# Optimization experiments

Hardware: AMD Instinct MI355X
Metric: run time of the kernel (lower is better)

The kernel has to match this reference:

```python
import jax, jax.numpy as jnp
import numpy as np

EMBED_DIM = 1024
NUM_HEADS = 16
HEAD_DIM = EMBED_DIM // NUM_HEADS
SCALING = HEAD_DIM ** -0.5


def setup_inputs() -> dict:
    key = jax.random.key(0)
    ks = jax.random.split(key, 10)
    B, S, D = 2, 2048, EMBED_DIM
    lim = 1.0 / np.sqrt(D)  # torch Linear default init scale
    def lin(k):
        kw, kb = jax.random.split(k)
        W = jax.random.uniform(kw, (D, D), jnp.float32, -lim, lim)
        b = jax.random.uniform(kb, (D,), jnp.float32, -lim, lim)
        return W, b
    Wq, bq = lin(ks[0])
    Wk, bk = lin(ks[1])
    Wv, bv = lin(ks[2])
    Wo, bo = lin(ks[3])
    hidden_states = jax.random.normal(ks[4], (B, S, D), jnp.float32)
    attention_mask = jnp.ones((B, S), jnp.int32)  # unused by the module's forward
    return {"hidden_states": hidden_states, "attention_mask": attention_mask,
            "Wq": Wq, "bq": bq, "Wk": Wk, "bk": bk, "Wv": Wv, "bv": bv,
            "Wo": Wo, "bo": bo}


def reference(hidden_states, attention_mask, Wq, bq, Wk, bk, Wv, bv, Wo, bo):
    B, S, D = hidden_states.shape
    H, hd = NUM_HEADS, HEAD_DIM

    def split_heads(x):  # [B,S,D] -> [B,H,S,hd]
        return x.reshape(B, S, H, hd).transpose(0, 2, 1, 3)

    q = split_heads(hidden_states @ Wq.T + bq) * SCALING
    k = split_heads(hidden_states @ Wk.T + bk)
    v = split_heads(hidden_states @ Wv.T + bv)

    scores = jnp.einsum("bhqd,bhkd->bhqk", q, k)  # [B,H,S,S]
    mask_value = jnp.finfo(scores.dtype).min
    causal = jnp.triu(jnp.ones((S, S), bool), k=1)  # True above diagonal
    scores = jnp.where(causal, mask_value, scores)
    probs = jax.nn.softmax(scores, axis=-1)

    out = jnp.einsum("bhqk,bhkd->bhqd", probs, v)  # [B,H,S,hd]
    out = out.transpose(0, 2, 1, 3).reshape(B, S, D)
    return out @ Wo.T + bo
```

## Files before the change

kernel.cpp:

```cpp
#include <hip/hip_runtime.h>


typedef __bf16 bf16;
typedef __attribute__((ext_vector_type(8))) __bf16 bf16x8;
typedef __attribute__((ext_vector_type(4))) __bf16 bf16x4;
typedef __attribute__((ext_vector_type(4))) float f32x4;

#define MFMA16(a, b, c) __builtin_amdgcn_mfma_f32_16x16x32_bf16((a), (b), (c), 0, 0, 0)

__device__ __forceinline__ void gl_lds16(const bf16* g, bf16* l) {
  __builtin_amdgcn_global_load_lds(
      (__attribute__((address_space(1))) void*)g,
      (__attribute__((address_space(3))) void*)l, 16, 0, 0);
}

__device__ __forceinline__ float exp2_raw(float x) {
  float r;
  asm("v_exp_f32 %0, %1" : "=v"(r) : "v"(x));
  return r;
}

__global__ __launch_bounds__(256) void cvt5(
    const float* __restrict__ x, const float* __restrict__ wq,
    const float* __restrict__ wk, const float* __restrict__ wv,
    const float* __restrict__ wo,
    bf16* __restrict__ xb, bf16* __restrict__ wqb, bf16* __restrict__ wkb,
    bf16* __restrict__ wvb, bf16* __restrict__ wob) {
  const int bx = blockIdx.x;
  const float* s;
  bf16* d;
  int base;
  if (bx < 4096)      { s = x;  d = xb;  base = bx; }
  else if (bx < 5120) { s = wq; d = wqb; base = bx - 4096; }
  else if (bx < 6144) { s = wk; d = wkb; base = bx - 5120; }
  else if (bx < 7168) { s = wv; d = wvb; base = bx - 6144; }
  else                { s = wo; d = wob; base = bx - 7168; }
  const int i = base * 1024 + threadIdx.x * 4;
  const float4 v = *(const float4*)(s + i);
  bf16x4 o;
  o[0] = (bf16)v.x; o[1] = (bf16)v.y; o[2] = (bf16)v.z; o[3] = (bf16)v.w;
  *(bf16x4*)(d + i) = o;
}

template <int BM, typename OutT>
__global__ __launch_bounds__(256, 2) void gemm_bt3(
    const bf16* __restrict__ A,
    const bf16* __restrict__ W0, const bf16* __restrict__ W1, const bf16* __restrict__ W2,
    const float* __restrict__ B0, const float* __restrict__ B1, const float* __restrict__ B2,
    OutT* __restrict__ O0, OutT* __restrict__ O1, OutT* __restrict__ O2,
    float s0, float s1, float s2, int K, int vt_which) {
  constexpr int WM = BM / 32;
  __shared__ bf16 As[BM * 64];
  __shared__ bf16 Bs[128 * 64];

  const int t = threadIdx.x;
  const int lane = t & 63;
  const int wv = t >> 6;
  const int wm = wv & 1, wn = wv >> 1;
  const int qd = lane >> 4, ln = lane & 15;

  const int which = blockIdx.x >> 3;
  const bf16* W = (which == 0) ? W0 : (which == 1) ? W1 : W2;
  const float* Bi = (which == 0) ? B0 : (which == 1) ? B1 : B2;
  OutT* O = (which == 0) ? O0 : (which == 1) ? O1 : O2;
  const float scale = (which == 0) ? s0 : (which == 1) ? s1 : s2;

  const int n0 = (blockIdx.x & 7) * 128;
  const int m0 = blockIdx.y * BM;

  f32x4 acc[WM][4] = {};

  for (int k0 = 0; k0 < K; k0 += 64) {
#pragma unroll
    for (int i = 0; i < BM / 32; ++i) {
      const int s = i * 256 + t;
      const int row = s >> 3;
      const int c = (s & 7) ^ (row & 7);
      gl_lds16(A + (size_t)(m0 + row) * K + k0 + c * 8, &As[s * 8]);
    }
#pragma unroll
    for (int i = 0; i < 4; ++i) {
      const int s = i * 256 + t;
      const int row = s >> 3;
      const int c = (s & 7) ^ (row & 7);
      gl_lds16(W + (size_t)(n0 + row) * K + k0 + c * 8, &Bs[s * 8]);
    }
    __syncthreads();

#pragma unroll
    for (int ks = 0; ks < 2; ++ks) {
      bf16x8 af[WM], bw[4];
#pragma unroll
      for (int i = 0; i < WM; ++i) {
        const int r = wm * (BM / 2) + i * 16 + ln;
        af[i] = *(const bf16x8*)&As[r * 64 + (((ks * 4 + qd) ^ (ln & 7)) << 3)];
      }
#pragma unroll
      for (int j = 0; j < 4; ++j) {
        const int r = wn * 64 + j * 16 + ln;
        bw[j] = *(const bf16x8*)&Bs[r * 64 + (((ks * 4 + qd) ^ (ln & 7)) << 3)];
      }
#pragma unroll
      for (int i = 0; i < WM; ++i)
#pragma unroll
        for (int j = 0; j < 4; ++j)
          acc[i][j] = MFMA16(af[i], bw[j], acc[i][j]);
    }
    __syncthreads();
  }

#pragma unroll
  for (int i = 0; i < WM; ++i) {
    const int row = m0 + wm * (BM / 2) + i * 16 + qd * 4;
#pragma unroll
    for (int j = 0; j < 4; ++j) {
      const int col = n0 + wn * 64 + j * 16 + ln;
      const float bias = Bi[col];
      if (which == vt_which) {
        const int bb = row >> 11, ss = row & 2047;
        const int hh = col >> 6, dd = col & 63;
        OutT* dst = O + ((size_t)((bb << 4) + hh) * 64 + dd) * 2048 + ss;
        if constexpr (sizeof(OutT) == 2) {
          bf16x4 pk;
#pragma unroll
          for (int r = 0; r < 4; ++r) pk[r] = (bf16)((acc[i][j][r] + bias) * scale);
          *(bf16x4*)dst = pk;
        } else {
#pragma unroll
          for (int r = 0; r < 4; ++r) dst[r] = (OutT)((acc[i][j][r] + bias) * scale);
        }
      } else {
#pragma unroll
        for (int r = 0; r < 4; ++r) {
          const float v = (acc[i][j][r] + bias) * scale;
          O[(size_t)(row + r) * 1024 + col] = (OutT)v;
        }
      }
    }
  }
}

__global__ __launch_bounds__(256, 4) void attn_causal(
    const bf16* __restrict__ Q, const bf16* __restrict__ Kg,
    const bf16* __restrict__ VT, bf16* __restrict__ Ob) {
  __shared__ bf16 Ks[2][64 * 64];
  __shared__ bf16 Vts[2][64 * 64];
  __shared__ bf16 Ps[4][16 * 64];

  const int t = threadIdx.x;
  const int lane = t & 63;
  const int w = t >> 6;
  const int qd = lane >> 4, ln = lane & 15;

  const int blk = blockIdx.x;
  const int bh = blk & 31;
  const int g = blk >> 5;
  const int a = g & 7, b = g >> 3;
  const int tq = (b == 0) ? (31 - a) : (b == 1) ? (16 + a) : (b == 2) ? (15 - a) : a;
  const int bb = bh >> 4, h = bh & 15;
  const size_t rowbase = (size_t)bb * 2048;
  const bf16* vtb = VT + (size_t)bh * 64 * 2048;

  const int q0 = tq * 64;
  const int nj = tq + 1;

  auto stage = [&](int buf, int j) {
    const bf16* kp = Kg + (rowbase + j * 64) * 1024 + h * 64;
#pragma unroll
    for (int i = 0; i < 2; ++i) {
      const int s = i * 256 + t;
      const int kv = s >> 3;
      const int c = (s & 7) ^ (kv & 7);
      gl_lds16(kp + (size_t)kv * 1024 + c * 8, &Ks[buf][s * 8]);
    }
#pragma unroll
    for (int i = 0; i < 2; ++i) {
      const int s = i * 256 + t;
      const int d = s >> 3;
      const int c = (s & 7) ^ (d & 7);
      gl_lds16(vtb + (size_t)d * 2048 + j * 64 + c * 8, &Vts[buf][s * 8]);
    }
  };

  const bf16* qp = Q + (rowbase + q0 + w * 16) * 1024 + h * 64;
  bf16x8 qf[2];
#pragma unroll
  for (int ks = 0; ks < 2; ++ks)
    qf[ks] = *(const bf16x8*)(qp + (size_t)ln * 1024 + ks * 32 + qd * 8);

  float l_run[4] = {0.f, 0.f, 0.f, 0.f};
  f32x4 accO[4] = {};

  stage(0, 0);

#pragma unroll 1
  for (int j = 0; j < nj; ++j) {
    const int buf = j & 1;
    __syncthreads();
    if (j + 1 < nj) stage(buf ^ 1, j + 1);

    f32x4 accS[4] = {};
    __builtin_amdgcn_s_setprio(1);
#pragma unroll
    for (int ks = 0; ks < 2; ++ks) {
#pragma unroll
      for (int nt = 0; nt < 4; ++nt) {
        const bf16x8 bk = *(const bf16x8*)
            &Ks[buf][(nt * 16 + ln) * 64 + (((ks * 4 + qd) ^ (ln & 7)) << 3)];
        accS[nt] = MFMA16(qf[ks], bk, accS[nt]);
      }
    }
    __builtin_amdgcn_s_setprio(0);

    if (j == nj - 1) {
#pragma unroll
      for (int r = 0; r < 4; ++r) {
        const int row = qd * 4 + r;
        const int qg = q0 + w * 16 + row;
        float sum = 0.f;
#pragma unroll
        for (int nt = 0; nt < 4; ++nt) {
          float p = exp2_raw(accS[nt][r]);
          const int col = nt * 16 + ln;
          if ((j * 64 + col) > qg) p = 0.f;
          sum += p;
          Ps[w][row * 64 + ((((col >> 3) ^ (row & 7))) << 3) + (col & 7)] = (bf16)p;
        }
        l_run[r] += sum;
      }
    } else {
#pragma unroll
      for (int r = 0; r < 4; ++r) {
        const int row = qd * 4 + r;
        float sum = 0.f;
#pragma unroll
        for (int nt = 0; nt < 4; ++nt) {
          const float p = exp2_raw(accS[nt][r]);
          const int col = nt * 16 + ln;
          sum += p;
          Ps[w][row * 64 + ((((col >> 3) ^ (row & 7))) << 3) + (col & 7)] = (bf16)p;
        }
        l_run[r] += sum;
      }
    }

    __builtin_amdgcn_s_setprio(1);
#pragma unroll
    for (int kt = 0; kt < 2; ++kt) {
      const bf16x8 ap = *(const bf16x8*)
          &Ps[w][ln * 64 + (((kt * 4 + qd) ^ (ln & 7)) << 3)];
#pragma unroll
      for (int nt = 0; nt < 4; ++nt) {
        const bf16x8 bv = *(const bf16x8*)
            &Vts[buf][(nt * 16 + ln) * 64 + (((kt * 4 + qd) ^ (ln & 7)) << 3)];
        accO[nt] = MFMA16(ap, bv, accO[nt]);
      }
    }
    __builtin_amdgcn_s_setprio(0);
  }

  bf16* op = Ob + (rowbase + q0 + w * 16) * 1024 + h * 64;
#pragma unroll
  for (int r = 0; r < 4; ++r) {
    float l = l_run[r];
#pragma unroll
    for (int off = 1; off < 16; off <<= 1) l += __shfl_xor(l, off, 64);
    const float inv_l = 1.0f / l;
#pragma unroll
    for (int nt = 0; nt < 4; ++nt)
      op[(size_t)(qd * 4 + r) * 1024 + nt * 16 + ln] = (bf16)(accO[nt][r] * inv_l);
  }
}

extern "C" void kernel_launch(void* const* d_in, const int* in_sizes, int n_in,
                              void* d_out, int out_size, void* d_ws, size_t ws_size,
                              hipStream_t stream) {
  const float* X  = (const float*)d_in[0];
  const float* Wq = (const float*)d_in[2];
  const float* bq = (const float*)d_in[3];
  const float* Wk = (const float*)d_in[4];
  const float* bk = (const float*)d_in[5];
  const float* Wv = (const float*)d_in[6];
  const float* bv = (const float*)d_in[7];
  const float* Wo = (const float*)d_in[8];
  const float* bo = (const float*)d_in[9];
  float* out = (float*)d_out;

  bf16* xb  = (bf16*)d_ws;
  bf16* wqb = xb  + (size_t)4096 * 1024;
  bf16* wkb = wqb + (size_t)1024 * 1024;
  bf16* wvb = wkb + (size_t)1024 * 1024;
  bf16* wob = wvb + (size_t)1024 * 1024;
  bf16* q   = wob + (size_t)1024 * 1024;
  bf16* k   = q   + (size_t)4096 * 1024;
  bf16* vt  = k   + (size_t)4096 * 1024;
  bf16* ao  = xb;

  const float scaling = 0.125f * 1.44269504088896f;

  dim3 blk(256);
  cvt5<<<dim3(8192), blk, 0, stream>>>(X, Wq, Wk, Wv, Wo, xb, wqb, wkb, wvb, wob);
  gemm_bt3<128, bf16><<<dim3(24, 32), blk, 0, stream>>>(
      xb, wqb, wkb, wvb, bq, bk, bv, q, k, vt, scaling, 1.f, 1.f, 1024, 2);
  attn_causal<<<dim3(1024), blk, 0, stream>>>(q, k, vt, ao);
  gemm_bt3<64, float><<<dim3(8, 64), blk, 0, stream>>>(
      ao, wob, wob, wob, bo, bo, bo, out, out, out, 1.f, 1.f, 1.f, 1024, -1);
}
```

Before: 183.8 us.

## Run causal attention as single-wave blocks reading K/V straight into registers

The attention kernel goes from 256-thread blocks, where four waves share double-buffered K and V^T tiles staged in LDS through async global-to-LDS loads, to 64-thread blocks. Each block now handles 16 query rows and loads its K and V^T fragments from global memory directly into registers, so LDS holds only the P tile. The grid grows to 4096 blocks and the heavy-first causal tile ordering is dropped. This removes the block barriers and LDS staging, but each K/V tile is now fetched four times as often through the cache. Load latency is no longer overlapped by the double buffer, and light blocks now launch before heavy ones, which can leave a long tail.

After: 266.7 us. 1.45x slower.

```diff
diff --git a/kernel.cpp b/kernel.cpp
--- a/kernel.cpp
+++ b/kernel.cpp
@@ -140,49 +140,26 @@
   }
 }
 
-__global__ __launch_bounds__(256, 4) void attn_causal(
+__global__ __launch_bounds__(64, 4) void attn_causal(
     const bf16* __restrict__ Q, const bf16* __restrict__ Kg,
     const bf16* __restrict__ VT, bf16* __restrict__ Ob) {
-  __shared__ bf16 Ks[2][64 * 64];
-  __shared__ bf16 Vts[2][64 * 64];
-  __shared__ bf16 Ps[4][16 * 64];
-
-  const int t = threadIdx.x;
-  const int lane = t & 63;
-  const int w = t >> 6;
+  __shared__ bf16 Ps[16 * 64];
+
+  const int lane = threadIdx.x;
   const int qd = lane >> 4, ln = lane & 15;
 
   const int blk = blockIdx.x;
   const int bh = blk & 31;
   const int g = blk >> 5;
-  const int a = g & 7, b = g >> 3;
-  const int tq = (b == 0) ? (31 - a) : (b == 1) ? (16 + a) : (b == 2) ? (15 - a) : a;
   const int bb = bh >> 4, h = bh & 15;
   const size_t rowbase = (size_t)bb * 2048;
+  const bf16* kb = Kg + rowbase * 1024 + h * 64;
   const bf16* vtb = VT + (size_t)bh * 64 * 2048;
 
-  const int q0 = tq * 64;
-  const int nj = tq + 1;
-
-  auto stage = [&](int buf, int j) {
-    const bf16* kp = Kg + (rowbase + j * 64) * 1024 + h * 64;
-#pragma unroll
-    for (int i = 0; i < 2; ++i) {
-      const int s = i * 256 + t;
-      const int kv = s >> 3;
-      const int c = (s & 7) ^ (kv & 7);
-      gl_lds16(kp + (size_t)kv * 1024 + c * 8, &Ks[buf][s * 8]);
-    }
-#pragma unroll
-    for (int i = 0; i < 2; ++i) {
-      const int s = i * 256 + t;
-      const int d = s >> 3;
-      const int c = (s & 7) ^ (d & 7);
-      gl_lds16(vtb + (size_t)d * 2048 + j * 64 + c * 8, &Vts[buf][s * 8]);
-    }
-  };
-
-  const bf16* qp = Q + (rowbase + q0 + w * 16) * 1024 + h * 64;
+  const int q0 = g * 16;
+  const int nj = (g >> 2) + 1;
+
+  const bf16* qp = Q + (rowbase + q0) * 1024 + h * 64;
   bf16x8 qf[2];
 #pragma unroll
   for (int ks = 0; ks < 2; ++ks)
@@ -191,32 +168,38 @@
   float l_run[4] = {0.f, 0.f, 0.f, 0.f};
   f32x4 accO[4] = {};
 
-  stage(0, 0);
-
 #pragma unroll 1
   for (int j = 0; j < nj; ++j) {
-    const int buf = j & 1;
-    __syncthreads();
-    if (j + 1 < nj) stage(buf ^ 1, j + 1);
+    bf16x8 bk[2][4];
+#pragma unroll
+    for (int ks = 0; ks < 2; ++ks)
+#pragma unroll
+      for (int nt = 0; nt < 4; ++nt)
+        bk[ks][nt] = *(const bf16x8*)
+            (kb + (size_t)(j * 64 + nt * 16 + ln) * 1024 + ks * 32 + qd * 8);
 
     f32x4 accS[4] = {};
     __builtin_amdgcn_s_setprio(1);
 #pragma unroll
-    for (int ks = 0; ks < 2; ++ks) {
-#pragma unroll
-      for (int nt = 0; nt < 4; ++nt) {
-        const bf16x8 bk = *(const bf16x8*)
-            &Ks[buf][(nt * 16 + ln) * 64 + (((ks * 4 + qd) ^ (ln & 7)) << 3)];
-        accS[nt] = MFMA16(qf[ks], bk, accS[nt]);
-      }
-    }
+    for (int ks = 0; ks < 2; ++ks)
+#pragma unroll
+      for (int nt = 0; nt < 4; ++nt)
+        accS[nt] = MFMA16(qf[ks], bk[ks][nt], accS[nt]);
     __builtin_amdgcn_s_setprio(0);
+
+    bf16x8 bv[2][4];
+#pragma unroll
+    for (int kt = 0; kt < 2; ++kt)
+#pragma unroll
+      for (int nt = 0; nt < 4; ++nt)
+        bv[kt][nt] = *(const bf16x8*)
+            (vtb + (size_t)(nt * 16 + ln) * 2048 + j * 64 + kt * 32 + qd * 8);
 
     if (j == nj - 1) {
 #pragma unroll
       for (int r = 0; r < 4; ++r) {
         const int row = qd * 4 + r;
-        const int qg = q0 + w * 16 + row;
+        const int qg = q0 + row;
         float sum = 0.f;
 #pragma unroll
         for (int nt = 0; nt < 4; ++nt) {
@@ -224,7 +207,7 @@
           const int col = nt * 16 + ln;
           if ((j * 64 + col) > qg) p = 0.f;
           sum += p;
-          Ps[w][row * 64 + ((((col >> 3) ^ (row & 7))) << 3) + (col & 7)] = (bf16)p;
+          Ps[row * 64 + ((((col >> 3) ^ (row & 7))) << 3) + (col & 7)] = (bf16)p;
         }
         l_run[r] += sum;
       }
@@ -238,7 +221,7 @@
           const float p = exp2_raw(accS[nt][r]);
           const int col = nt * 16 + ln;
           sum += p;
-          Ps[w][row * 64 + ((((col >> 3) ^ (row & 7))) << 3) + (col & 7)] = (bf16)p;
+          Ps[row * 64 + ((((col >> 3) ^ (row & 7))) << 3) + (col & 7)] = (bf16)p;
         }
         l_run[r] += sum;
       }
@@ -248,18 +231,15 @@
 #pragma unroll
     for (int kt = 0; kt < 2; ++kt) {
       const bf16x8 ap = *(const bf16x8*)
-          &Ps[w][ln * 64 + (((kt * 4 + qd) ^ (ln & 7)) << 3)];
-#pragma unroll
-      for (int nt = 0; nt < 4; ++nt) {
-        const bf16x8 bv = *(const bf16x8*)
-            &Vts[buf][(nt * 16 + ln) * 64 + (((kt * 4 + qd) ^ (ln & 7)) << 3)];
-        accO[nt] = MFMA16(ap, bv, accO[nt]);
-      }
+          &Ps[ln * 64 + (((kt * 4 + qd) ^ (ln & 7)) << 3)];
+#pragma unroll
+      for (int nt = 0; nt < 4; ++nt)
+        accO[nt] = MFMA16(ap, bv[kt][nt], accO[nt]);
     }
     __builtin_amdgcn_s_setprio(0);
   }
 
-  bf16* op = Ob + (rowbase + q0 + w * 16) * 1024 + h * 64;
+  bf16* op = Ob + (rowbase + q0) * 1024 + h * 64;
 #pragma unroll
   for (int r = 0; r < 4; ++r) {
     float l = l_run[r];
@@ -302,7 +282,7 @@
   cvt5<<<dim3(8192), blk, 0, stream>>>(X, Wq, Wk, Wv, Wo, xb, wqb, wkb, wvb, wob);
   gemm_bt3<128, bf16><<<dim3(24, 32), blk, 0, stream>>>(
       xb, wqb, wkb, wvb, bq, bk, bv, q, k, vt, scaling, 1.f, 1.f, 1024, 2);
-  attn_causal<<<dim3(1024), blk, 0, stream>>>(q, k, vt, ao);
+  attn_causal<<<dim3(4096), dim3(64), 0, stream>>>(q, k, vt, ao);
   gemm_bt3<64, float><<<dim3(8, 64), blk, 0, stream>>>(
       ao, wob, wob, wob, bo, bo, bo, out, out, out, 1.f, 1.f, 1.f, 1024, -1);
 }
```

## Keep attention probabilities in registers via transposed S and permlane swaps

Applied to the files above, without the earlier changes.

The QK^T MFMA now computes the transposed score tile, so each lane holds one query row's scores across several keys. The probabilities are packed to bf16 and rearranged with permlane swaps directly into the A-operand layout for the PV MFMA. This removes the LDS round trip through the Ps buffer and simplifies the row-sum reduction. In exchange it adds cross-lane permute instructions and depends on the operand-layout mapping being exactly right.

Result: faster. 174.5 us (-5.0%).

```diff
diff --git a/kernel.cpp b/kernel.cpp
--- a/kernel.cpp
+++ b/kernel.cpp
@@ -5,6 +5,7 @@
 typedef __attribute__((ext_vector_type(8))) __bf16 bf16x8;
 typedef __attribute__((ext_vector_type(4))) __bf16 bf16x4;
 typedef __attribute__((ext_vector_type(4))) float f32x4;
+typedef __attribute__((ext_vector_type(4))) unsigned int u32x4;
 
 #define MFMA16(a, b, c) __builtin_amdgcn_mfma_f32_16x16x32_bf16((a), (b), (c), 0, 0, 0)
 
@@ -145,7 +146,6 @@
     const bf16* __restrict__ VT, bf16* __restrict__ Ob) {
   __shared__ bf16 Ks[2][64 * 64];
   __shared__ bf16 Vts[2][64 * 64];
-  __shared__ bf16 Ps[4][16 * 64];
 
   const int t = threadIdx.x;
   const int lane = t & 63;
@@ -188,7 +188,7 @@
   for (int ks = 0; ks < 2; ++ks)
     qf[ks] = *(const bf16x8*)(qp + (size_t)ln * 1024 + ks * 32 + qd * 8);
 
-  float l_run[4] = {0.f, 0.f, 0.f, 0.f};
+  float l_run = 0.f;
   f32x4 accO[4] = {};
 
   stage(0, 0);
@@ -199,7 +199,7 @@
     __syncthreads();
     if (j + 1 < nj) stage(buf ^ 1, j + 1);
 
-    f32x4 accS[4] = {};
+    f32x4 accT[4] = {};
     __builtin_amdgcn_s_setprio(1);
 #pragma unroll
     for (int ks = 0; ks < 2; ++ks) {
@@ -207,68 +207,77 @@
       for (int nt = 0; nt < 4; ++nt) {
         const bf16x8 bk = *(const bf16x8*)
             &Ks[buf][(nt * 16 + ln) * 64 + (((ks * 4 + qd) ^ (ln & 7)) << 3)];
-        accS[nt] = MFMA16(qf[ks], bk, accS[nt]);
+        accT[nt] = MFMA16(bk, qf[ks], accT[nt]);
       }
     }
     __builtin_amdgcn_s_setprio(0);
 
+    float p[4][4];
     if (j == nj - 1) {
-#pragma unroll
-      for (int r = 0; r < 4; ++r) {
-        const int row = qd * 4 + r;
-        const int qg = q0 + w * 16 + row;
-        float sum = 0.f;
-#pragma unroll
-        for (int nt = 0; nt < 4; ++nt) {
-          float p = exp2_raw(accS[nt][r]);
-          const int col = nt * 16 + ln;
-          if ((j * 64 + col) > qg) p = 0.f;
-          sum += p;
-          Ps[w][row * 64 + ((((col >> 3) ^ (row & 7))) << 3) + (col & 7)] = (bf16)p;
+      const int qg = q0 + w * 16 + ln;
+#pragma unroll
+      for (int nt = 0; nt < 4; ++nt)
+#pragma unroll
+        for (int r = 0; r < 4; ++r) {
+          float pv = exp2_raw(accT[nt][r]);
+          const int kv = j * 64 + nt * 16 + qd * 4 + r;
+          if (kv > qg) pv = 0.f;
+          p[nt][r] = pv;
+          l_run += pv;
         }
-        l_run[r] += sum;
-      }
     } else {
 #pragma unroll
-      for (int r = 0; r < 4; ++r) {
-        const int row = qd * 4 + r;
-        float sum = 0.f;
-#pragma unroll
-        for (int nt = 0; nt < 4; ++nt) {
-          const float p = exp2_raw(accS[nt][r]);
-          const int col = nt * 16 + ln;
-          sum += p;
-          Ps[w][row * 64 + ((((col >> 3) ^ (row & 7))) << 3) + (col & 7)] = (bf16)p;
+      for (int nt = 0; nt < 4; ++nt)
+#pragma unroll
+        for (int r = 0; r < 4; ++r) {
+          const float pv = exp2_raw(accT[nt][r]);
+          p[nt][r] = pv;
+          l_run += pv;
         }
-        l_run[r] += sum;
-      }
+    }
+
+    unsigned int wd[2][4];
+#pragma unroll
+    for (int kt = 0; kt < 2; ++kt) {
+      unsigned int L0, H0, L1, H1;
+      asm("v_cvt_pk_bf16_f32 %0, %1, %2" : "=v"(L0) : "v"(p[2 * kt][0]), "v"(p[2 * kt][1]));
+      asm("v_cvt_pk_bf16_f32 %0, %1, %2" : "=v"(H0) : "v"(p[2 * kt][2]), "v"(p[2 * kt][3]));
+      asm("v_cvt_pk_bf16_f32 %0, %1, %2" : "=v"(L1) : "v"(p[2 * kt + 1][0]), "v"(p[2 * kt + 1][1]));
+      asm("v_cvt_pk_bf16_f32 %0, %1, %2" : "=v"(H1) : "v"(p[2 * kt + 1][2]), "v"(p[2 * kt + 1][3]));
+      asm("v_permlane32_swap_b32 %0, %1" : "+v"(L0), "+v"(L1));
+      asm("v_permlane16_swap_b32 %0, %1" : "+v"(L0), "+v"(L1));
+      asm("v_permlane32_swap_b32 %0, %1" : "+v"(H0), "+v"(H1));
+      asm("v_permlane16_swap_b32 %0, %1" : "+v"(H0), "+v"(H1));
+      wd[kt][0] = L0; wd[kt][1] = H0; wd[kt][2] = L1; wd[kt][3] = H1;
     }
 
     __builtin_amdgcn_s_setprio(1);
 #pragma unroll
     for (int kt = 0; kt < 2; ++kt) {
-      const bf16x8 ap = *(const bf16x8*)
-          &Ps[w][ln * 64 + (((kt * 4 + qd) ^ (ln & 7)) << 3)];
+      const u32x4 uw = {wd[kt][0], wd[kt][1], wd[kt][2], wd[kt][3]};
+      const bf16x8 pa = __builtin_bit_cast(bf16x8, uw);
 #pragma unroll
       for (int nt = 0; nt < 4; ++nt) {
         const bf16x8 bv = *(const bf16x8*)
             &Vts[buf][(nt * 16 + ln) * 64 + (((kt * 4 + qd) ^ (ln & 7)) << 3)];
-        accO[nt] = MFMA16(ap, bv, accO[nt]);
+        accO[nt] = MFMA16(pa, bv, accO[nt]);
       }
     }
     __builtin_amdgcn_s_setprio(0);
   }
 
+  float l = l_run;
+  l += __shfl_xor(l, 16, 64);
+  l += __shfl_xor(l, 32, 64);
+  const float inv = 1.0f / l;
+
   bf16* op = Ob + (rowbase + q0 + w * 16) * 1024 + h * 64;
 #pragma unroll
   for (int r = 0; r < 4; ++r) {
-    float l = l_run[r];
-#pragma unroll
-    for (int off = 1; off < 16; off <<= 1) l += __shfl_xor(l, off, 64);
-    const float inv_l = 1.0f / l;
+    const float inv_r = __shfl(inv, (lane >> 4) * 4 + r, 64);
 #pragma unroll
     for (int nt = 0; nt < 4; ++nt)
-      op[(size_t)(qd * 4 + r) * 1024 + nt * 16 + ln] = (bf16)(accO[nt][r] * inv_l);
+      op[(size_t)(qd * 4 + r) * 1024 + nt * 16 + ln] = (bf16)(accO[nt][r] * inv_r);
   }
 }
 
```
